# Performance work log

Hardware: AMD Instinct MI355X
Metric: run time of the kernel (lower is better)

The kernel has to match this reference:

```python
import jax, jax.numpy as jnp
import numpy as np

N_BLOCKS = 96
N = N_BLOCKS ** 2          # number of image blocks = n_blocks^2
D = 1024                   # feature dim (fixed by Linear(1024+1, 128))
EPS_COS = 1e-6             # eps of F.cosine_similarity
EPS_BN = 1e-5              # BatchNorm1d eps


def setup_inputs() -> dict:
    key = jax.random.key(0)
    ks = jax.random.split(key, 6)
    return {
        "features": jax.random.normal(ks[0], (N, D), dtype=jnp.float32),
        "scores": jax.random.uniform(ks[1], (N,), dtype=jnp.float32),
        "W1": jax.random.normal(ks[2], (D + 1, 128), dtype=jnp.float32) * 0.03,
        "b1": jnp.zeros((128,), jnp.float32),
        "g1": jnp.ones((128,), jnp.float32),
        "be1": jnp.zeros((128,), jnp.float32),
        "W2": jax.random.normal(ks[3], (128, 64), dtype=jnp.float32) * 0.08,
        "b2": jnp.zeros((64,), jnp.float32),
        "g2": jnp.ones((64,), jnp.float32),
        "be2": jnp.zeros((64,), jnp.float32),
        "W3": jax.random.normal(ks[4], (64, 1), dtype=jnp.float32) * 0.12,
        "b3": jnp.zeros((1,), jnp.float32),
    }


def _gaussian_similarity(features):
    # Vectorized form of the O(N^2) pairwise loop:
    #   cos_ij = <f_i, f_j> / max(|f_i||f_j|, eps)
    #   sigma^2 = D * (0.5 + 0.5 * cos)  ->  2*sigma^2 = D * (1 + cos)
    #   sim_ij = exp(-|f_i - f_j|^2 / (2*sigma^2)),  sim_ii = 1
    sq = jnp.sum(features * features, axis=-1)          # [N] squared norms
    gram = features @ features.T                          # [N, N] big GEMM
    norms = jnp.sqrt(sq)
    cos = gram / jnp.maximum(norms[:, None] * norms[None, :], EPS_COS)
    d2 = jnp.maximum(sq[:, None] + sq[None, :] - 2.0 * gram, 0.0)
    denom = jnp.maximum(jnp.float32(D) * (1.0 + cos), EPS_COS)
    sim = jnp.exp(-d2 / denom)
    eye = jnp.eye(sim.shape[0], dtype=bool)
    return jnp.where(eye, jnp.float32(1.0), sim)


def _bn_eval(h, gamma, beta):
    # BatchNorm1d in eval mode with init running stats (mean=0, var=1).
    return gamma * (h / jnp.sqrt(1.0 + EPS_BN)) + beta


def reference(features, scores, W1, b1, g1, be1, W2, b2, g2, be2, W3, b3):
    sim = _gaussian_similarity(features)                  # [N, N]
    x = jnp.concatenate([features, scores[:, None]], axis=1)  # [N, D+1]
    h = jax.nn.relu(_bn_eval(x @ W1 + b1, g1, be1))       # [N, 128]
    h = jax.nn.relu(_bn_eval(h @ W2 + b2, g2, be2))       # [N, 64]
    agg = jax.nn.sigmoid(h @ W3 + b3)[:, 0]               # [N]
    sim_mean = jnp.mean(sim, axis=1)                      # [N]
    # Torch broadcast [N,1] * [N] -> [N,N], then .mean() == mean(agg)*mean(sim_mean)
    return jnp.mean(agg) * jnp.mean(sim_mean)


if __name__ == "__main__":
    out = reference(**setup_inputs())
    print(out)
```

## Files before the change

kernel.cpp:

```cpp
#include <hip/hip_runtime.h>

#define N_IMG 9216
#define DFEAT 1024
#define NBR 72
#define NPAIR 1332

typedef __attribute__((ext_vector_type(8))) short short8;
typedef __attribute__((ext_vector_type(4))) float floatx4;
typedef __attribute__((ext_vector_type(16))) float floatx16;
typedef __attribute__((ext_vector_type(4))) int intx4;
typedef __attribute__((ext_vector_type(8))) int intx8;

#define C1F 0.0014088818759657845f
#define C2F 0.05308355472172724f

__device__ __forceinline__ void async_copy16(const void* g, void* l) {
  __builtin_amdgcn_global_load_lds((const __attribute__((address_space(1))) void*)g,
                                   (__attribute__((address_space(3))) void*)l,
                                   16, 0, 0);
}

__device__ __forceinline__ unsigned short f2bf(float x) {
  union { float f; unsigned u; } a; a.f = x;
  unsigned u = a.u;
  u += 0x7fffu + ((u >> 16) & 1u);
  return (unsigned short)(u >> 16);
}

__device__ __forceinline__ size_t sw_src(int P) {
  int L = P >> 3, s = P & 7;
  int row = 2 * L + (s & 1);
  int c = ((s >> 1) - L) & 3;
  return (size_t)row * DFEAT + (size_t)c * 16;
}
__device__ __forceinline__ intx4 ld16s(const unsigned char* base, int r, int c) {
  int L = r >> 1;
  int slot = (((c + L) & 3) << 1) | (r & 1);
  return *(const intx4*)(base + L * 128 + slot * 16);
}
__device__ __forceinline__ intx8 ldfrags(const unsigned char* base, int r, int kh) {
  intx4 lo = ld16s(base, r, kh * 2);
  intx4 hi = ld16s(base, r, kh * 2 + 1);
  intx8 v;
  v[0] = lo[0]; v[1] = lo[1]; v[2] = lo[2]; v[3] = lo[3];
  v[4] = hi[0]; v[5] = hi[1]; v[6] = hi[2]; v[7] = hi[3];
  return v;
}

__global__ __launch_bounds__(256) void convert_prep(const float* __restrict__ f,
                                                    const float* __restrict__ W1,
                                                    unsigned char* __restrict__ fb8,
                                                    float* __restrict__ sL,
                                                    float* __restrict__ pL,
                                                    unsigned short* __restrict__ W1t,
                                                    double* __restrict__ sums) {
  int b = blockIdx.x, t = threadIdx.x;
  if (b < 2304) {
    int lane = t & 63, wave = t >> 6;
    int row = b * 4 + wave;
    const float4* src = (const float4*)f + (size_t)row * 256;
    unsigned int* dst = (unsigned int*)(fb8 + (size_t)row * DFEAT);
    float4 v0 = src[lane], v1 = src[64 + lane], v2 = src[128 + lane], v3 = src[192 + lane];
    float s = v0.x * v0.x + v0.y * v0.y + v0.z * v0.z + v0.w * v0.w
            + v1.x * v1.x + v1.y * v1.y + v1.z * v1.z + v1.w * v1.w
            + v2.x * v2.x + v2.y * v2.y + v2.z * v2.z + v2.w * v2.w
            + v3.x * v3.x + v3.y * v3.y + v3.z * v3.z + v3.w * v3.w;
#pragma unroll
    for (int off = 32; off > 0; off >>= 1) s += __shfl_xor(s, off, 64);
    float rinv = rsqrtf(s);
    float4 vv[4] = {v0, v1, v2, v3};
#pragma unroll
    for (int j = 0; j < 4; j++) {
      float4 v = vv[j];
      int pk = __builtin_amdgcn_cvt_pk_fp8_f32(v.x * rinv, v.y * rinv, 0, false);
      pk = __builtin_amdgcn_cvt_pk_fp8_f32(v.z * rinv, v.w * rinv, pk, true);
      dst[j * 64 + lane] = (unsigned int)pk;
    }
    if (lane == 0) {
      sL[row] = s * C1F;
      pL[row] = sqrtf(s) * C2F;
    }
  } else {
    int j = b - 2304;
    if (j == 0 && t < 2) sums[t] = 0.0;
    for (int k = t; k < DFEAT; k += 256)
      W1t[(size_t)j * DFEAT + k] = f2bf(W1[(size_t)k * 128 + j]);
  }
}

__global__ __launch_bounds__(256, 2) void gram_sim(const unsigned char* __restrict__ fb8,
                                                   const float* __restrict__ sL,
                                                   const float* __restrict__ pL,
                                                   double* __restrict__ sums) {
  int rem = blockIdx.x, bcol = 0;
  for (;;) {
    int mlim = 2 * bcol + 2; if (mlim > NBR) mlim = NBR;
    if (rem < mlim) break;
    rem -= mlim; bcol++;
  }
  int brow = rem;

  __shared__ __align__(16) unsigned char Ab[2][8192];
  __shared__ __align__(16) unsigned char Bb[2][16384];
  __shared__ float sA[128], pA[128], sB[256], pB[256];
  __shared__ float wpart[4];

  int t = threadIdx.x, lane = t & 63, wave = t >> 6;
  if (t < 128) { sA[t] = sL[brow * 128 + t]; pA[t] = pL[brow * 128 + t]; }
  sB[t] = sL[bcol * 256 + t];
  pB[t] = pL[bcol * 256 + t];

  const unsigned char* Asrc = fb8 + (size_t)brow * 128 * DFEAT;
  const unsigned char* Bsrc = fb8 + (size_t)bcol * 256 * DFEAT;

  const size_t d0 = sw_src(t);
  const size_t d1 = sw_src(t + 256);
  const size_t d2 = sw_src(t + 512);
  const size_t d3 = sw_src(t + 768);

  floatx16 acc[2][4];
#pragma unroll
  for (int mi = 0; mi < 2; mi++)
#pragma unroll
    for (int ni = 0; ni < 4; ni++)
#pragma unroll
      for (int e = 0; e < 16; e++) acc[mi][ni][e] = 0.f;

  const int wr = (wave & 1) * 64, wc = (wave >> 1) * 128;
  const int r32 = lane & 31, kh = lane >> 5;

  async_copy16(Asrc + d0, &Ab[0][t * 16]);
  async_copy16(Asrc + d1, &Ab[0][(t + 256) * 16]);
  async_copy16(Bsrc + d0, &Bb[0][t * 16]);
  async_copy16(Bsrc + d1, &Bb[0][(t + 256) * 16]);
  async_copy16(Bsrc + d2, &Bb[0][(t + 512) * 16]);
  async_copy16(Bsrc + d3, &Bb[0][(t + 768) * 16]);

  for (int kb = 0; kb < 16; kb++) {
    __syncthreads();
    if (kb < 15) {
      const int nb = (kb + 1) & 1;
      const size_t k0 = (size_t)(kb + 1) * 64;
      async_copy16(Asrc + d0 + k0, &Ab[nb][t * 16]);
      async_copy16(Asrc + d1 + k0, &Ab[nb][(t + 256) * 16]);
      async_copy16(Bsrc + d0 + k0, &Bb[nb][t * 16]);
      async_copy16(Bsrc + d1 + k0, &Bb[nb][(t + 256) * 16]);
      async_copy16(Bsrc + d2 + k0, &Bb[nb][(t + 512) * 16]);
      async_copy16(Bsrc + d3 + k0, &Bb[nb][(t + 768) * 16]);
    }
    const unsigned char* Ac = Ab[kb & 1];
    const unsigned char* Bc = Bb[kb & 1];
    intx8 a[2], b[4];
#pragma unroll
    for (int mi = 0; mi < 2; mi++) a[mi] = ldfrags(Ac, wr + mi * 32 + r32, kh);
#pragma unroll
    for (int ni = 0; ni < 4; ni++) b[ni] = ldfrags(Bc, wc + ni * 32 + r32, kh);
#pragma unroll
    for (int mi = 0; mi < 2; mi++)
#pragma unroll
      for (int ni = 0; ni < 4; ni++)
        acc[mi][ni] = __builtin_amdgcn_mfma_scale_f32_32x32x64_f8f6f4(
            a[mi], b[ni], acc[mi][ni], 0, 0, 0, 0x7F7F7F7F, 0, 0x7F7F7F7F);
  }

  const bool interior = (brow < 2 * bcol);
  float lsum = 0.f;
#pragma unroll
  for (int ni = 0; ni < 4; ni++) {
    int j_loc = wc + ni * 32 + r32;
    float sj = sB[j_loc], pj = pB[j_loc];
    int j_g = bcol * 256 + j_loc;
#pragma unroll
    for (int mi = 0; mi < 2; mi++) {
      int rbase = wr + mi * 32 + 4 * kh;
#pragma unroll
      for (int reg = 0; reg < 16; reg++) {
        int i_loc = rbase + (reg & 3) + 8 * (reg >> 2);
        float u = acc[mi][ni][reg];
        float si = sA[i_loc], pi = pA[i_loc];
        float r = __builtin_amdgcn_rcpf(1.f + u);
        float del = pi * pj;
        float gam = si + sj + del;
        float sim = __builtin_amdgcn_exp2f(fmaf(-gam, r, del));
        if (interior) {
          lsum += sim;
        } else {
          int i_g = brow * 128 + i_loc;
          lsum += (i_g < j_g) ? 2.f * sim : (i_g == j_g ? 1.f : 0.f);
        }
      }
    }
  }
  if (interior) lsum *= 2.f;
#pragma unroll
  for (int off = 32; off > 0; off >>= 1) lsum += __shfl_down(lsum, off, 64);
  if (lane == 0) wpart[wave] = lsum;
  __syncthreads();
  if (t == 0)
    atomicAdd(&sums[0], (double)(wpart[0] + wpart[1] + wpart[2] + wpart[3]));
}

__global__ __launch_bounds__(256) void mlp_full(const float* __restrict__ f,
                                                const unsigned short* __restrict__ W1t,
                                                const float* __restrict__ scores,
                                                const float* __restrict__ W1,
                                                const float* __restrict__ b1,
                                                const float* __restrict__ g1,
                                                const float* __restrict__ be1,
                                                const float* __restrict__ W2, const float* __restrict__ b2,
                                                const float* __restrict__ g2, const float* __restrict__ be2,
                                                const float* __restrict__ W3, const float* __restrict__ b3,
                                                double* __restrict__ sums) {
  int r0 = blockIdx.x * 32;

  __shared__ __align__(16) float As32[32 * 32];
  __shared__ __align__(16) unsigned short Bs[128 * 32];
  __shared__ float h1s[32][128];
  __shared__ float h2s[32][65];
  __shared__ float sc[32], b1s[128], g1s[128], be1s[128], wls[128], ls[32];

  int t = threadIdx.x, lane = t & 63, wave = t >> 6;
  if (t < 32) sc[t] = scores[r0 + t];
  if (t < 128) {
    b1s[t] = b1[t]; g1s[t] = g1[t]; be1s[t] = be1[t];
    wls[t] = W1[(size_t)DFEAT * 128 + t];
  }

  floatx4 acc[4];
#pragma unroll
  for (int b = 0; b < 4; b++) acc[b] = (floatx4){0.f, 0.f, 0.f, 0.f};

  const int wr = (wave & 1) * 16, wc = (wave >> 1) * 64;

  for (int k0 = 0; k0 < DFEAT; k0 += 32) {
    __syncthreads();
    {
      int rA = t >> 3, p = t & 7, l = p ^ (rA & 7);
      async_copy16(f + (size_t)(r0 + rA) * DFEAT + k0 + l * 4, (char*)As32 + t * 16);
      int c = t, rB = c >> 2; p = c & 3; l = p ^ (rB & 3);
      async_copy16(W1t + (size_t)rB * DFEAT + k0 + l * 8, (char*)Bs + c * 16);
      c = t + 256; rB = c >> 2; p = c & 3; l = p ^ (rB & 3);
      async_copy16(W1t + (size_t)rB * DFEAT + k0 + l * 8, (char*)Bs + c * 16);
    }
    __syncthreads();

    const int mrow = lane & 15, kq = (lane >> 4) * 8;
    short8 a, b[4];
    {
      int row = wr + mrow;
      int l0 = kq >> 2;
      int p0 = l0 ^ (row & 7), p1 = (l0 + 1) ^ (row & 7);
      float4 f0 = *(const float4*)&As32[row * 32 + p0 * 4];
      float4 f1 = *(const float4*)&As32[row * 32 + p1 * 4];
      a[0] = (short)f2bf(f0.x); a[1] = (short)f2bf(f0.y);
      a[2] = (short)f2bf(f0.z); a[3] = (short)f2bf(f0.w);
      a[4] = (short)f2bf(f1.x); a[5] = (short)f2bf(f1.y);
      a[6] = (short)f2bf(f1.z); a[7] = (short)f2bf(f1.w);
    }
#pragma unroll
    for (int nt = 0; nt < 4; nt++) {
      int row = wc + nt * 16 + mrow;
      int p = (kq >> 3) ^ (row & 3);
      b[nt] = *(const short8*)&Bs[row * 32 + p * 8];
    }
#pragma unroll
    for (int nt = 0; nt < 4; nt++)
      acc[nt] = __builtin_amdgcn_mfma_f32_16x16x32_bf16(a, b[nt], acc[nt], 0, 0, 0);
  }

  const float inv = 1.0f / sqrtf(1.0f + 1e-5f);
  const int rq = (lane >> 4) * 4, cn = lane & 15;
#pragma unroll
  for (int nt = 0; nt < 4; nt++) {
    int j = wc + nt * 16 + cn;
    float bj = b1s[j], gj = g1s[j] * inv, bej = be1s[j], wj = wls[j];
#pragma unroll
    for (int rr = 0; rr < 4; rr++) {
      int iL = wr + rq + rr;
      float pre = acc[nt][rr] + sc[iL] * wj + bj;
      h1s[iL][j] = fmaxf(gj * pre + bej, 0.f);
    }
  }
  __syncthreads();

  {
    int j = t & 63, rg = (t >> 6) * 8;
    float a2[8];
#pragma unroll
    for (int rr = 0; rr < 8; rr++) a2[rr] = 0.f;
    for (int k = 0; k < 128; k++) {
      float w = W2[k * 64 + j];
#pragma unroll
      for (int rr = 0; rr < 8; rr++) a2[rr] = fmaf(h1s[rg + rr][k], w, a2[rr]);
    }
    float scv = g2[j] * inv, bi = b2[j], be = be2[j];
#pragma unroll
    for (int rr = 0; rr < 8; rr++)
      h2s[rg + rr][j] = fmaxf(scv * (a2[rr] + bi) + be, 0.f);
  }
  __syncthreads();

  if (t < 32) {
    float z = b3[0];
#pragma unroll
    for (int k = 0; k < 64; k++) z = fmaf(h2s[t][k], W3[k], z);
    ls[t] = 1.f / (1.f + __expf(-z));
  }
  __syncthreads();
  if (t == 0) {
    float s = 0.f;
#pragma unroll
    for (int iL = 0; iL < 32; iL++) s += ls[iL];
    atomicAdd(&sums[1], (double)s);
  }
}

__global__ void finalize(const double* __restrict__ sums, float* __restrict__ out) {
  double simmean = sums[0] / ((double)N_IMG * (double)N_IMG);
  double aggmean = sums[1] / (double)N_IMG;
  out[0] = (float)(aggmean * simmean);
}

extern "C" void kernel_launch(void* const* d_in, const int* in_sizes, int n_in,
                              void* d_out, int out_size, void* d_ws, size_t ws_size,
                              hipStream_t stream) {
  const float* f      = (const float*)d_in[0];
  const float* scores = (const float*)d_in[1];
  const float* W1 = (const float*)d_in[2];
  const float* b1 = (const float*)d_in[3];
  const float* g1 = (const float*)d_in[4];
  const float* be1 = (const float*)d_in[5];
  const float* W2 = (const float*)d_in[6];
  const float* b2 = (const float*)d_in[7];
  const float* g2 = (const float*)d_in[8];
  const float* be2 = (const float*)d_in[9];
  const float* W3 = (const float*)d_in[10];
  const float* b3 = (const float*)d_in[11];

  char* ws = (char*)d_ws;
  unsigned char* fb8  = (unsigned char*)ws;
  float* sL           = (float*)(ws + 9437184);
  float* pL           = (float*)(ws + 9474048);
  unsigned short* W1t = (unsigned short*)(ws + 9510912);
  double* sums        = (double*)(ws + 9773056);

  convert_prep<<<2432, 256, 0, stream>>>(f, W1, fb8, sL, pL, W1t, sums);
  gram_sim<<<NPAIR, 256, 0, stream>>>(fb8, sL, pL, sums);
  mlp_full<<<288, 256, 0, stream>>>(f, W1t, scores, W1, b1, g1, be1,
                                    W2, b2, g2, be2, W3, b3, sums);
  finalize<<<1, 1, 0, stream>>>(sums, (float*)d_out);
}
```

Baseline: 198.3 us.

## Quantize features to FP4 in MFMA-ready layout and load directly from global

Replaces FP8 normalized features with a hand-rolled FP4 (e2m1) quantization scaled by 32, stored in a pre-tiled layout that matches MFMA fragment order. The Gram kernel drops the LDS double buffer and reads fragments straight from global into registers with software prefetch, using the FP4 mode of the scaled MFMA. It also remaps block indices to spread work across XCDs, and adjusts the epilogue for the new scale. This halves the bytes moved and raises MFMA throughput, but FP4 coarsens the Gram values and so the similarity values, and it gives up LDS reuse.

```diff
diff --git a/kernel.cpp b/kernel.cpp
--- a/kernel.cpp
+++ b/kernel.cpp
@@ -27,29 +27,30 @@
   return (unsigned short)(u >> 16);
 }
 
-__device__ __forceinline__ size_t sw_src(int P) {
-  int L = P >> 3, s = P & 7;
-  int row = 2 * L + (s & 1);
-  int c = ((s >> 1) - L) & 3;
-  return (size_t)row * DFEAT + (size_t)c * 16;
-}
-__device__ __forceinline__ intx4 ld16s(const unsigned char* base, int r, int c) {
-  int L = r >> 1;
-  int slot = (((c + L) & 3) << 1) | (r & 1);
-  return *(const intx4*)(base + L * 128 + slot * 16);
-}
-__device__ __forceinline__ intx8 ldfrags(const unsigned char* base, int r, int kh) {
-  intx4 lo = ld16s(base, r, kh * 2);
-  intx4 hi = ld16s(base, r, kh * 2 + 1);
-  intx8 v;
-  v[0] = lo[0]; v[1] = lo[1]; v[2] = lo[2]; v[3] = lo[3];
-  v[4] = hi[0]; v[5] = hi[1]; v[6] = hi[2]; v[7] = hi[3];
-  return v;
+__device__ __forceinline__ unsigned q4(float z) {
+  unsigned sg = (__float_as_uint(z) >> 28) & 8u;
+  float a = fabsf(z);
+  unsigned c = (a < 0.25f) ? 0u : (a < 0.75f) ? 1u : (a < 1.25f) ? 2u :
+               (a < 1.75f) ? 3u : (a < 2.5f)  ? 4u : (a < 3.5f)  ? 5u :
+               (a < 5.0f)  ? 6u : 7u;
+  return c | sg;
+}
+__device__ __forceinline__ unsigned short pk4(float4 v, float sc) {
+  unsigned b0 = q4(v.x * sc) | (q4(v.y * sc) << 4);
+  unsigned b1 = q4(v.z * sc) | (q4(v.w * sc) << 4);
+  return (unsigned short)(b0 | (b1 << 8));
+}
+
+__device__ __forceinline__ intx8 ext8(intx4 v) {
+  intx8 r;
+  r[0] = v[0]; r[1] = v[1]; r[2] = v[2]; r[3] = v[3];
+  r[4] = 0; r[5] = 0; r[6] = 0; r[7] = 0;
+  return r;
 }
 
 __global__ __launch_bounds__(256) void convert_prep(const float* __restrict__ f,
                                                     const float* __restrict__ W1,
-                                                    unsigned char* __restrict__ fb8,
+                                                    unsigned char* __restrict__ fbT,
                                                     float* __restrict__ sL,
                                                     float* __restrict__ pL,
                                                     unsigned short* __restrict__ W1t,
@@ -59,7 +60,6 @@
     int lane = t & 63, wave = t >> 6;
     int row = b * 4 + wave;
     const float4* src = (const float4*)f + (size_t)row * 256;
-    unsigned int* dst = (unsigned int*)(fb8 + (size_t)row * DFEAT);
     float4 v0 = src[lane], v1 = src[64 + lane], v2 = src[128 + lane], v3 = src[192 + lane];
     float s = v0.x * v0.x + v0.y * v0.y + v0.z * v0.z + v0.w * v0.w
             + v1.x * v1.x + v1.y * v1.y + v1.z * v1.z + v1.w * v1.w
@@ -67,15 +67,15 @@
             + v3.x * v3.x + v3.y * v3.y + v3.z * v3.z + v3.w * v3.w;
 #pragma unroll
     for (int off = 32; off > 0; off >>= 1) s += __shfl_xor(s, off, 64);
-    float rinv = rsqrtf(s);
-    float4 vv[4] = {v0, v1, v2, v3};
-#pragma unroll
-    for (int j = 0; j < 4; j++) {
-      float4 v = vv[j];
-      int pk = __builtin_amdgcn_cvt_pk_fp8_f32(v.x * rinv, v.y * rinv, 0, false);
-      pk = __builtin_amdgcn_cvt_pk_fp8_f32(v.z * rinv, v.w * rinv, pk, true);
-      dst[j * 64 + lane] = (unsigned int)pk;
-    }
+    float zsc = rsqrtf(s) * 32.f;
+    unsigned short u0 = pk4(v0, zsc), u1 = pk4(v1, zsc),
+                   u2 = pk4(v2, zsc), u3 = pk4(v3, zsc);
+    unsigned char* tb = fbT + (size_t)(row >> 5) * 16384 + (row & 31) * 32 + (lane & 15) * 2;
+    int ko = (lane >> 4) * 1024;
+    *(unsigned short*)(tb + ko) = u0;
+    *(unsigned short*)(tb + ko + 4096) = u1;
+    *(unsigned short*)(tb + ko + 8192) = u2;
+    *(unsigned short*)(tb + ko + 12288) = u3;
     if (lane == 0) {
       sL[row] = s * C1F;
       pL[row] = sqrtf(s) * C2F;
@@ -88,11 +88,13 @@
   }
 }
 
-__global__ __launch_bounds__(256, 2) void gram_sim(const unsigned char* __restrict__ fb8,
+__global__ __launch_bounds__(256, 2) void gram_sim(const unsigned char* __restrict__ fbT,
                                                    const float* __restrict__ sL,
                                                    const float* __restrict__ pL,
                                                    double* __restrict__ sums) {
-  int rem = blockIdx.x, bcol = 0;
+  int x = blockIdx.x & 7, ii = blockIdx.x >> 3;
+  int L = (x < 4) ? x * 167 + ii : 668 + (x - 4) * 166 + ii;
+  int rem = L, bcol = 0;
   for (;;) {
     int mlim = 2 * bcol + 2; if (mlim > NBR) mlim = NBR;
     if (rem < mlim) break;
@@ -100,8 +102,6 @@
   }
   int brow = rem;
 
-  __shared__ __align__(16) unsigned char Ab[2][8192];
-  __shared__ __align__(16) unsigned char Bb[2][16384];
   __shared__ float sA[128], pA[128], sB[256], pB[256];
   __shared__ float wpart[4];
 
@@ -109,58 +109,56 @@
   if (t < 128) { sA[t] = sL[brow * 128 + t]; pA[t] = pL[brow * 128 + t]; }
   sB[t] = sL[bcol * 256 + t];
   pB[t] = pL[bcol * 256 + t];
-
-  const unsigned char* Asrc = fb8 + (size_t)brow * 128 * DFEAT;
-  const unsigned char* Bsrc = fb8 + (size_t)bcol * 256 * DFEAT;
-
-  const size_t d0 = sw_src(t);
-  const size_t d1 = sw_src(t + 256);
-  const size_t d2 = sw_src(t + 512);
-  const size_t d3 = sw_src(t + 768);
-
-  floatx16 acc[2][4];
-#pragma unroll
-  for (int mi = 0; mi < 2; mi++)
-#pragma unroll
-    for (int ni = 0; ni < 4; ni++)
-#pragma unroll
-      for (int e = 0; e < 16; e++) acc[mi][ni][e] = 0.f;
+  __syncthreads();
 
   const int wr = (wave & 1) * 64, wc = (wave >> 1) * 128;
   const int r32 = lane & 31, kh = lane >> 5;
-
-  async_copy16(Asrc + d0, &Ab[0][t * 16]);
-  async_copy16(Asrc + d1, &Ab[0][(t + 256) * 16]);
-  async_copy16(Bsrc + d0, &Bb[0][t * 16]);
-  async_copy16(Bsrc + d1, &Bb[0][(t + 256) * 16]);
-  async_copy16(Bsrc + d2, &Bb[0][(t + 512) * 16]);
-  async_copy16(Bsrc + d3, &Bb[0][(t + 768) * 16]);
-
+  const int loff = r32 * 32 + kh * 16;
+
+  const unsigned char* pa0 = fbT + (size_t)(brow * 4 + (wr >> 5)) * 16384 + loff;
+  const unsigned char* pa1 = pa0 + 16384;
+  const unsigned char* pb0 = fbT + (size_t)(bcol * 8 + (wc >> 5)) * 16384 + loff;
+  const unsigned char* pb1 = pb0 + 16384;
+  const unsigned char* pb2 = pb0 + 32768;
+  const unsigned char* pb3 = pb0 + 49152;
+
+  floatx16 acc[2][4];
+#pragma unroll
+  for (int mi = 0; mi < 2; mi++)
+#pragma unroll
+    for (int ni = 0; ni < 4; ni++)
+#pragma unroll
+      for (int e = 0; e < 16; e++) acc[mi][ni][e] = 0.f;
+
+  intx4 aC[2], bC[4], aN[2], bN[4];
+  aC[0] = *(const intx4*)pa0; aC[1] = *(const intx4*)pa1;
+  bC[0] = *(const intx4*)pb0; bC[1] = *(const intx4*)pb1;
+  bC[2] = *(const intx4*)pb2; bC[3] = *(const intx4*)pb3;
+
+#pragma unroll
   for (int kb = 0; kb < 16; kb++) {
-    __syncthreads();
+    const int o = (kb + 1) * 1024;
     if (kb < 15) {
-      const int nb = (kb + 1) & 1;
-      const size_t k0 = (size_t)(kb + 1) * 64;
-      async_copy16(Asrc + d0 + k0, &Ab[nb][t * 16]);
-      async_copy16(Asrc + d1 + k0, &Ab[nb][(t + 256) * 16]);
-      async_copy16(Bsrc + d0 + k0, &Bb[nb][t * 16]);
-      async_copy16(Bsrc + d1 + k0, &Bb[nb][(t + 256) * 16]);
-      async_copy16(Bsrc + d2 + k0, &Bb[nb][(t + 512) * 16]);
-      async_copy16(Bsrc + d3 + k0, &Bb[nb][(t + 768) * 16]);
-    }
-    const unsigned char* Ac = Ab[kb & 1];
-    const unsigned char* Bc = Bb[kb & 1];
-    intx8 a[2], b[4];
-#pragma unroll
-    for (int mi = 0; mi < 2; mi++) a[mi] = ldfrags(Ac, wr + mi * 32 + r32, kh);
-#pragma unroll
-    for (int ni = 0; ni < 4; ni++) b[ni] = ldfrags(Bc, wc + ni * 32 + r32, kh);
+      aN[0] = *(const intx4*)(pa0 + o); aN[1] = *(const intx4*)(pa1 + o);
+      bN[0] = *(const intx4*)(pb0 + o); bN[1] = *(const intx4*)(pb1 + o);
+      bN[2] = *(const intx4*)(pb2 + o); bN[3] = *(const intx4*)(pb3 + o);
+    }
+    intx8 A8[2], B8[4];
+#pragma unroll
+    for (int mi = 0; mi < 2; mi++) A8[mi] = ext8(aC[mi]);
+#pragma unroll
+    for (int ni = 0; ni < 4; ni++) B8[ni] = ext8(bC[ni]);
 #pragma unroll
     for (int mi = 0; mi < 2; mi++)
 #pragma unroll
       for (int ni = 0; ni < 4; ni++)
         acc[mi][ni] = __builtin_amdgcn_mfma_scale_f32_32x32x64_f8f6f4(
-            a[mi], b[ni], acc[mi][ni], 0, 0, 0, 0x7F7F7F7F, 0, 0x7F7F7F7F);
+            A8[mi], B8[ni], acc[mi][ni], 4, 4,
+            0, 0x7F7F7F7F, 0, 0x7F7F7F7F);
+#pragma unroll
+    for (int mi = 0; mi < 2; mi++) aC[mi] = aN[mi];
+#pragma unroll
+    for (int ni = 0; ni < 4; ni++) bC[ni] = bN[ni];
   }
 
   const bool interior = (brow < 2 * bcol);
@@ -176,12 +174,13 @@
 #pragma unroll
       for (int reg = 0; reg < 16; reg++) {
         int i_loc = rbase + (reg & 3) + 8 * (reg >> 2);
-        float u = acc[mi][ni][reg];
+        float g = acc[mi][ni][reg];
         float si = sA[i_loc], pi = pA[i_loc];
-        float r = __builtin_amdgcn_rcpf(1.f + u);
+        float r = __builtin_amdgcn_rcpf(1024.f + g);
         float del = pi * pj;
         float gam = si + sj + del;
-        float sim = __builtin_amdgcn_exp2f(fmaf(-gam, r, del));
+        float tt = gam * r;
+        float sim = __builtin_amdgcn_exp2f(fmaf(-1024.f, tt, del));
         if (interior) {
           lsum += sim;
         } else {
@@ -338,14 +337,14 @@
   const float* b3 = (const float*)d_in[11];
 
   char* ws = (char*)d_ws;
-  unsigned char* fb8  = (unsigned char*)ws;
-  float* sL           = (float*)(ws + 9437184);
-  float* pL           = (float*)(ws + 9474048);
-  unsigned short* W1t = (unsigned short*)(ws + 9510912);
-  double* sums        = (double*)(ws + 9773056);
-
-  convert_prep<<<2432, 256, 0, stream>>>(f, W1, fb8, sL, pL, W1t, sums);
-  gram_sim<<<NPAIR, 256, 0, stream>>>(fb8, sL, pL, sums);
+  unsigned char* fbT  = (unsigned char*)ws;
+  float* sL           = (float*)(ws + 4718592);
+  float* pL           = (float*)(ws + 4755456);
+  unsigned short* W1t = (unsigned short*)(ws + 4792320);
+  double* sums        = (double*)(ws + 5054464);
+
+  convert_prep<<<2432, 256, 0, stream>>>(f, W1, fbT, sL, pL, W1t, sums);
+  gram_sim<<<NPAIR, 256, 0, stream>>>(fbT, sL, pL, sums);
   mlp_full<<<288, 256, 0, stream>>>(f, W1t, scores, W1, b1, g1, be1,
                                     W2, b2, g2, be2, W3, b3, sums);
   finalize<<<1, 1, 0, stream>>>(sums, (float*)d_out);
```

Measured after the change: 183.9 us. 1.08x faster.
